# Kernel optimization log

Hardware: AMD Instinct MI355X
Metric: run time of the kernel (lower is better)

## Reference

```python
import jax, jax.numpy as jnp
import numpy as np


def _grid_sample_points(feat, gx, gy):
    """Bilinear grid_sample at point list, align_corners=False, zeros padding.
    feat: [B, H, W, C]; gx, gy: [B, N] normalized coords in [-1, 1].
    Returns [B, N, C].
    """
    B, H, W, C = feat.shape
    # unnormalize (align_corners=False): -1 -> -0.5, +1 -> size-0.5
    ix = (gx + 1.0) * (W * 0.5) - 0.5
    iy = (gy + 1.0) * (H * 0.5) - 0.5
    x0 = jnp.floor(ix)
    y0 = jnp.floor(iy)
    x1 = x0 + 1.0
    y1 = y0 + 1.0
    wx1 = ix - x0
    wx0 = 1.0 - wx1
    wy1 = iy - y0
    wy0 = 1.0 - wy1
    bidx = jnp.arange(B)[:, None]  # [B,1] broadcasts against [B,N]

    def gather(yy, xx):
        valid = (xx >= 0) & (xx <= W - 1) & (yy >= 0) & (yy <= H - 1)
        xi = jnp.clip(xx, 0, W - 1).astype(jnp.int32)
        yi = jnp.clip(yy, 0, H - 1).astype(jnp.int32)
        v = feat[bidx, yi, xi]  # [B, N, C]
        return v * valid[..., None].astype(feat.dtype)

    out = (gather(y0, x0) * (wy0 * wx0)[..., None]
           + gather(y0, x1) * (wy0 * wx1)[..., None]
           + gather(y1, x0) * (wy1 * wx0)[..., None]
           + gather(y1, x1) * (wy1 * wx1)[..., None])
    return out


def setup_inputs() -> dict:
    key = jax.random.key(0)
    k1, k2, k3, k4, k5 = jax.random.split(key, 5)
    B, C, T, Wd, Hd = 16, 64, 16, 36, 36
    N, D = 4096, C * T  # num_neurons, num_input
    x = jax.random.normal(k1, (B, C, T, Wd, Hd), dtype=jnp.float32)
    mu = jax.random.uniform(k2, (N, 2), minval=-1.0, maxval=1.0, dtype=jnp.float32)
    sigma = jax.random.uniform(k3, (N,), dtype=jnp.float32)  # unused in eval mode
    W = jax.random.normal(k4, (N, D), dtype=jnp.float32) * 0.02
    b = jax.random.normal(k5, (N,), dtype=jnp.float32) * 0.01
    return {"x": x, "mu": mu, "sigma": sigma, "W": W, "b": b}


def reference(x, mu, sigma, W, b):
    # eval-mode forward (self.training == False): grid = mu broadcast over batch
    B, C, T, Wd, Hd = x.shape
    N = mu.shape[0]
    # torch: x.view(B, C*T, Wd, Hd); grid_sample treats dim2 as H_in, dim3 as W_in
    feat = x.reshape(B, C * T, Wd, Hd).transpose(0, 2, 3, 1)
    g = jnp.clip(mu, -1.0, 1.0)
    gx = jnp.broadcast_to(g[:, 0], (B, N))  # grid[...,0] indexes W_in
    gy = jnp.broadcast_to(g[:, 1], (B, N))  # grid[...,1] indexes H_in
    sampled = _grid_sample_points(feat, gx, gy)  # [B, N, C*T]
    # PoissonLinearReadout 3D path == per-neuron dot product (diagonal of full matmul)
    y = jnp.einsum('bnc,nc->bn', sampled, W) + b
    return jax.nn.elu(y) + 1.0
```

## Files before the change

kernel.cpp:

```cpp
#include <hip/hip_runtime.h>
#include <hip/hip_bf16.h>
#include <cmath>

#define CT    1024
#define PIX   1296
#define BATCH 16
#define NNEUR 4096
#define HW    36
#define NBINS (HW * HW)
#define NB    4
#define BQ    4
#define BCT   (BATCH * CT)

#if defined(__has_builtin)
#  if __has_builtin(__builtin_amdgcn_fdot2_f32_bf16)
#    define HAVE_FDOT2_BF16 1
#  endif
#endif
#ifndef HAVE_FDOT2_BF16
#  define HAVE_FDOT2_BF16 0
#endif

typedef __bf16 bf16x2 __attribute__((ext_vector_type(2)));
__device__ __forceinline__ bf16x2 as_bf16x2(unsigned u) {
    union { unsigned u; bf16x2 v; } cv; cv.u = u; return cv.v;
}

__device__ __forceinline__ unsigned short bfu(float f) {
    __hip_bfloat16 h = __float2bfloat16(f);
    return *reinterpret_cast<unsigned short*>(&h);
}
__device__ __forceinline__ float bflo(unsigned u) { return __uint_as_float(u << 16); }
__device__ __forceinline__ float bfhi(unsigned u) { return __uint_as_float(u & 0xFFFF0000u); }

__global__ __launch_bounds__(256) void transpose_bf16_kernel(
    const float* __restrict__ x, __hip_bfloat16* __restrict__ feat)
{
    __shared__ unsigned short lds[64][34];
    const int b      = blockIdx.z;
    const int ctBase = blockIdx.y * 64;
    const int pBase  = blockIdx.x * 32;
    const int t      = threadIdx.x;
    const size_t xb  = (size_t)b * CT * PIX;
    {
        const int r  = t >> 2;
        const int pc = (t & 3) * 8;
        const float* src = x + xb + (size_t)(ctBase + r) * PIX + pBase + pc;
        if (pBase + 32 <= PIX) {
            float4 a = reinterpret_cast<const float4*>(src)[0];
            float4 c = reinterpret_cast<const float4*>(src)[1];
            lds[r][pc + 0] = bfu(a.x); lds[r][pc + 1] = bfu(a.y);
            lds[r][pc + 2] = bfu(a.z); lds[r][pc + 3] = bfu(a.w);
            lds[r][pc + 4] = bfu(c.x); lds[r][pc + 5] = bfu(c.y);
            lds[r][pc + 6] = bfu(c.z); lds[r][pc + 7] = bfu(c.w);
        } else {
#pragma unroll
            for (int i = 0; i < 8; ++i) {
                int p = pBase + pc + i;
                lds[r][pc + i] = (p < PIX) ? bfu(src[i]) : (unsigned short)0;
            }
        }
    }
    __syncthreads();
    const int pr = t >> 3;
    const int cc = (t & 7) * 8;
    if (pBase + pr < PIX) {
        unsigned short o[8];
#pragma unroll
        for (int i = 0; i < 8; ++i) o[i] = lds[cc + i][pr];
        const size_t off = ((size_t)(pBase + pr) * BATCH + b) * CT + ctBase + cc;
        *reinterpret_cast<uint4*>((unsigned short*)feat + off) = *reinterpret_cast<uint4*>(o);
    }
}

__global__ __launch_bounds__(1024) void sortpack_kernel(
    const float* __restrict__ mu, int* __restrict__ perm,
    const float* __restrict__ W, __hip_bfloat16* __restrict__ Wb)
{
    const int t = threadIdx.x;
    if (blockIdx.x != 0) {
        const int i = (blockIdx.x - 1) * 1024 + t;
        const float4 v = reinterpret_cast<const float4*>(W)[i];
        unsigned short o[4] = { bfu(v.x), bfu(v.y), bfu(v.z), bfu(v.w) };
        reinterpret_cast<ushort4*>(Wb)[i] = *reinterpret_cast<ushort4*>(o);
        return;
    }

    __shared__ int hist[NBINS];
    __shared__ int chunkSum[48];
    for (int i = t; i < NBINS; i += 1024) hist[i] = 0;
    __syncthreads();

    int key[4];
#pragma unroll
    for (int j = 0; j < 4; ++j) {
        const int n = t + j * 1024;
        float gx = fminf(fmaxf(mu[2 * n],     -1.f), 1.f);
        float gy = fminf(fmaxf(mu[2 * n + 1], -1.f), 1.f);
        float ix = (gx + 1.f) * (HW * 0.5f) - 0.5f;
        float iy = (gy + 1.f) * (HW * 0.5f) - 0.5f;
        int xi = min(max((int)floorf(ix), 0), HW - 1);
        int yi = min(max((int)floorf(iy), 0), HW - 1);
        key[j] = yi * HW + xi;
        atomicAdd(&hist[key[j]], 1);
    }
    __syncthreads();
    if (t < 41) {
        int s = 0;
        for (int i = 0; i < 32; ++i) {
            int idx = t * 32 + i;
            if (idx < NBINS) s += hist[idx];
        }
        chunkSum[t] = s;
    }
    __syncthreads();
    if (t == 0) {
        int run = 0;
        for (int i = 0; i < 41; ++i) { int v = chunkSum[i]; chunkSum[i] = run; run += v; }
    }
    __syncthreads();
    if (t < 41) {
        int run = chunkSum[t];
        for (int i = 0; i < 32; ++i) {
            int idx = t * 32 + i;
            if (idx < NBINS) { int v = hist[idx]; hist[idx] = run; run += v; }
        }
    }
    __syncthreads();
#pragma unroll
    for (int j = 0; j < 4; ++j) {
        const int n = t + j * 1024;
        const int pos = atomicAdd(&hist[key[j]], 1);
        perm[pos] = n;
    }
}

__global__ __launch_bounds__(256) void readout_bf16_kernel(
    const __hip_bfloat16* __restrict__ feat,
    const float* __restrict__ mu,
    const __hip_bfloat16* __restrict__ Wb,
    const float* __restrict__ bias,
    const int* __restrict__ perm,
    float* __restrict__ out)
{
    const int bid = blockIdx.x;
    const int xcd = bid & 7;
    const int r   = bid >> 3;
    const int g   = xcd * 128 + (r >> 2);
    const int q   = r & 3;
    const int t = threadIdx.x;
    const int c = t & 127;
    const int h = t >> 7;

    const int4 nids = *reinterpret_cast<const int4*>(perm + g * NB);
    const int nid[NB] = { nids.x, nids.y, nids.z, nids.w };

    uint4 wq[NB];
#pragma unroll
    for (int nb = 0; nb < NB; ++nb)
        wq[nb] = reinterpret_cast<const uint4*>(Wb + (size_t)nid[nb] * CT)[c];

#if !HAVE_FDOT2_BF16
    float w[NB][8];
#pragma unroll
    for (int nb = 0; nb < NB; ++nb) {
        w[nb][0] = bflo(wq[nb].x); w[nb][1] = bfhi(wq[nb].x);
        w[nb][2] = bflo(wq[nb].y); w[nb][3] = bfhi(wq[nb].y);
        w[nb][4] = bflo(wq[nb].z); w[nb][5] = bfhi(wq[nb].z);
        w[nb][6] = bflo(wq[nb].w); w[nb][7] = bfhi(wq[nb].w);
    }
#endif

    __shared__ float wmat16[16][NB];
    __shared__ int   upix[16];
    __shared__ float uw[16][NB];
    __shared__ int   ucount_s;

    if (t < 16) {
#pragma unroll
        for (int j = 0; j < NB; ++j) wmat16[t][j] = 0.f;
    }

    int   mypix = -1;
    float mycw  = 0.f;
    if (t < 16) {
        const int nb = t >> 2, k = t & 3;
        const int n = nid[nb];
        float gx = fminf(fmaxf(mu[2 * n],     -1.f), 1.f);
        float gy = fminf(fmaxf(mu[2 * n + 1], -1.f), 1.f);
        float ix = (gx + 1.f) * (HW * 0.5f) - 0.5f;
        float iy = (gy + 1.f) * (HW * 0.5f) - 0.5f;
        float x0f = floorf(ix), y0f = floorf(iy);
        float wx1 = ix - x0f, wx0 = 1.f - wx1;
        float wy1 = iy - y0f, wy0 = 1.f - wy1;
        int xx = (int)x0f + (k & 1), yy = (int)y0f + (k >> 1);
        bool valid = (xx >= 0) && (xx < HW) && (yy >= 0) && (yy < HW);
        int xi = min(max(xx, 0), HW - 1), yi = min(max(yy, 0), HW - 1);
        mypix = yi * HW + xi;
        mycw  = ((k & 1) ? wx1 : wx0) * ((k >> 1) ? wy1 : wy0) * (valid ? 1.f : 0.f);
    }

    int myslot = 15;
#pragma unroll
    for (int j = 15; j >= 0; --j) {
        int pj = __shfl(mypix, j, 64);
        if (pj == mypix) myslot = j;
    }
    if (t < 16) atomicAdd(&wmat16[myslot][t >> 2], mycw);

    const bool uniq = (t < 16) && (myslot == t);
    const unsigned long long mask = __ballot(uniq);
    if (t == 0) ucount_s = __popcll(mask);
    const int pix0 = __shfl(mypix, 0, 64);
    __syncthreads();

    const int U    = ucount_s;
    const int Upad = (U + 3) & ~3;
    if (uniq) {
        const int pos = __popcll(mask & ((1ull << t) - 1));
        upix[pos] = mypix;
#pragma unroll
        for (int j = 0; j < NB; ++j) uw[pos][j] = wmat16[t][j];
    }
    if (t >= U && t < Upad) {
        upix[t] = pix0;
#pragma unroll
        for (int j = 0; j < NB; ++j) uw[t][j] = 0.f;
    }
    __syncthreads();

    float acc[NB][2];
#pragma unroll
    for (int nb = 0; nb < NB; ++nb) { acc[nb][0] = 0.f; acc[nb][1] = 0.f; }

    const int b0 = q * BQ + h * 2;
    const unsigned short* fb = (const unsigned short*)feat + (size_t)b0 * CT + (size_t)c * 8;

    for (int u = 0; u < Upad; u += 4) {
        int poff[4];
#pragma unroll
        for (int s = 0; s < 4; ++s) poff[s] = upix[u + s] * BCT;
        uint4 va[4], vb[4];
#pragma unroll
        for (int s = 0; s < 4; ++s) {
            va[s] = *reinterpret_cast<const uint4*>(fb + poff[s]);
            vb[s] = *reinterpret_cast<const uint4*>(fb + poff[s] + CT);
        }
#pragma unroll
        for (int s = 0; s < 4; ++s) {
            const float4 pw = *reinterpret_cast<const float4*>(uw[u + s]);
            const float pws[NB] = { pw.x, pw.y, pw.z, pw.w };
#if HAVE_FDOT2_BF16
#pragma unroll
            for (int nb = 0; nb < NB; ++nb) {
                if (pws[nb] != 0.f) {
                    float d0 = __builtin_amdgcn_fdot2_f32_bf16(as_bf16x2(va[s].x), as_bf16x2(wq[nb].x), 0.f, false);
                    float d1 = __builtin_amdgcn_fdot2_f32_bf16(as_bf16x2(vb[s].x), as_bf16x2(wq[nb].x), 0.f, false);
                    d0 = __builtin_amdgcn_fdot2_f32_bf16(as_bf16x2(va[s].y), as_bf16x2(wq[nb].y), d0, false);
                    d1 = __builtin_amdgcn_fdot2_f32_bf16(as_bf16x2(vb[s].y), as_bf16x2(wq[nb].y), d1, false);
                    d0 = __builtin_amdgcn_fdot2_f32_bf16(as_bf16x2(va[s].z), as_bf16x2(wq[nb].z), d0, false);
                    d1 = __builtin_amdgcn_fdot2_f32_bf16(as_bf16x2(vb[s].z), as_bf16x2(wq[nb].z), d1, false);
                    d0 = __builtin_amdgcn_fdot2_f32_bf16(as_bf16x2(va[s].w), as_bf16x2(wq[nb].w), d0, false);
                    d1 = __builtin_amdgcn_fdot2_f32_bf16(as_bf16x2(vb[s].w), as_bf16x2(wq[nb].w), d1, false);
                    acc[nb][0] = fmaf(pws[nb], d0, acc[nb][0]);
                    acc[nb][1] = fmaf(pws[nb], d1, acc[nb][1]);
                }
            }
#else
            float fa[8] = { bflo(va[s].x), bfhi(va[s].x), bflo(va[s].y), bfhi(va[s].y),
                            bflo(va[s].z), bfhi(va[s].z), bflo(va[s].w), bfhi(va[s].w) };
            float fbv[8] = { bflo(vb[s].x), bfhi(vb[s].x), bflo(vb[s].y), bfhi(vb[s].y),
                             bflo(vb[s].z), bfhi(vb[s].z), bflo(vb[s].w), bfhi(vb[s].w) };
#pragma unroll
            for (int nb = 0; nb < NB; ++nb) {
                if (pws[nb] != 0.f) {
                    float d0 = fa[0]  * w[nb][0];
                    float d1 = fbv[0] * w[nb][0];
#pragma unroll
                    for (int j = 1; j < 8; ++j) {
                        d0 = fmaf(fa[j],  w[nb][j], d0);
                        d1 = fmaf(fbv[j], w[nb][j], d1);
                    }
                    acc[nb][0] = fmaf(pws[nb], d0, acc[nb][0]);
                    acc[nb][1] = fmaf(pws[nb], d1, acc[nb][1]);
                }
            }
#endif
        }
    }

    __shared__ float red[4][NB][2];
#pragma unroll
    for (int nb = 0; nb < NB; ++nb) {
#pragma unroll
        for (int i = 0; i < 2; ++i) {
            float v = acc[nb][i];
#pragma unroll
            for (int off = 32; off > 0; off >>= 1)
                v += __shfl_down(v, off, 64);
            acc[nb][i] = v;
        }
    }
    const int wave = t >> 6, lane = t & 63;
    if (lane == 0) {
#pragma unroll
        for (int nb = 0; nb < NB; ++nb) {
            red[wave][nb][0] = acc[nb][0];
            red[wave][nb][1] = acc[nb][1];
        }
    }
    __syncthreads();
    if (t < NB * BQ) {
        const int nb = t >> 2, bl = t & 3;
        const int hh = bl >> 1, i = bl & 1;
        float y = red[hh * 2][nb][i] + red[hh * 2 + 1][nb][i] + bias[nid[nb]];
        const int b = q * BQ + bl;
        out[(size_t)b * NNEUR + nid[nb]] = (y > 0.f) ? (y + 1.f) : expf(y);
    }
}

__global__ __launch_bounds__(256) void readout_f32_strided_kernel(
    const float* __restrict__ x,
    const float* __restrict__ mu,
    const float* __restrict__ Wm,
    const float* __restrict__ bias,
    float* __restrict__ out)
{
    const int n = blockIdx.x;
    const int t = threadIdx.x;
    const float4 w4 = reinterpret_cast<const float4*>(Wm + (size_t)n * CT)[t];
    float gx = fminf(fmaxf(mu[2 * n],     -1.f), 1.f);
    float gy = fminf(fmaxf(mu[2 * n + 1], -1.f), 1.f);
    float ix = (gx + 1.f) * (HW * 0.5f) - 0.5f;
    float iy = (gy + 1.f) * (HW * 0.5f) - 0.5f;
    float x0f = floorf(ix), y0f = floorf(iy);
    float wx1 = ix - x0f, wx0 = 1.f - wx1;
    float wy1 = iy - y0f, wy0 = 1.f - wy1;
    int x0 = (int)x0f, y0 = (int)y0f;
    float cw[4]; int cp[4];
#pragma unroll
    for (int k = 0; k < 4; ++k) {
        int xx = x0 + (k & 1), yy = y0 + (k >> 1);
        bool valid = (xx >= 0) && (xx < HW) && (yy >= 0) && (yy < HW);
        int xi = min(max(xx, 0), HW - 1), yi = min(max(yy, 0), HW - 1);
        cp[k] = yi * HW + xi;
        cw[k] = ((k & 1) ? wx1 : wx0) * ((k >> 1) ? wy1 : wy0) * (valid ? 1.f : 0.f);
    }
    float acc[BATCH];
#pragma unroll
    for (int b = 0; b < BATCH; ++b) {
        float s = 0.f;
#pragma unroll
        for (int k = 0; k < 4; ++k) {
            if (cw[k] != 0.f) {
                const float* fp = x + (size_t)b * CT * PIX + cp[k];
                const int c0 = 4 * t;
                s += cw[k] * (fp[(size_t)(c0 + 0) * PIX] * w4.x
                            + fp[(size_t)(c0 + 1) * PIX] * w4.y
                            + fp[(size_t)(c0 + 2) * PIX] * w4.z
                            + fp[(size_t)(c0 + 3) * PIX] * w4.w);
            }
        }
        acc[b] = s;
    }
#pragma unroll
    for (int b = 0; b < BATCH; ++b) {
        float v = acc[b];
#pragma unroll
        for (int off = 32; off > 0; off >>= 1)
            v += __shfl_down(v, off, 64);
        acc[b] = v;
    }
    __shared__ float red[4][BATCH];
    const int wave = t >> 6, lane = t & 63;
    if (lane == 0) {
#pragma unroll
        for (int b = 0; b < BATCH; ++b) red[wave][b] = acc[b];
    }
    __syncthreads();
    if (t < BATCH) {
        float y = red[0][t] + red[1][t] + red[2][t] + red[3][t] + bias[n];
        out[(size_t)t * NNEUR + n] = (y > 0.f) ? (y + 1.f) : expf(y);
    }
}

extern "C" void kernel_launch(void* const* d_in, const int* in_sizes, int n_in,
                              void* d_out, int out_size, void* d_ws, size_t ws_size,
                              hipStream_t stream)
{
    const float* x    = (const float*)d_in[0];
    const float* mu   = (const float*)d_in[1];
    const float* Wm   = (const float*)d_in[3];
    const float* bias = (const float*)d_in[4];
    float* out = (float*)d_out;

    const size_t featBytes = (size_t)BATCH * PIX * CT * sizeof(__hip_bfloat16);
    const size_t wBytes    = (size_t)NNEUR * CT * sizeof(__hip_bfloat16);
    const size_t permBytes = (size_t)NNEUR * sizeof(int);
    if (ws_size >= featBytes + wBytes + permBytes) {
        __hip_bfloat16* feat = (__hip_bfloat16*)d_ws;
        __hip_bfloat16* Wb   = (__hip_bfloat16*)((char*)d_ws + featBytes);
        int* perm = (int*)((char*)d_ws + featBytes + wBytes);
        dim3 tg((PIX + 31) / 32, CT / 64, BATCH);
        transpose_bf16_kernel<<<tg, 256, 0, stream>>>(x, feat);
        sortpack_kernel<<<1 + NNEUR * CT / 4 / 1024, 1024, 0, stream>>>(mu, perm, Wm, Wb);
        readout_bf16_kernel<<<(NNEUR / NB) * (BATCH / BQ), 256, 0, stream>>>(
            feat, mu, Wb, bias, perm, out);
    } else {
        readout_f32_strided_kernel<<<NNEUR, 256, 0, stream>>>(x, mu, Wm, bias, out);
    }
}
```

Measured before the change: 58.71 us.

## Merge transpose and sort/pack into one staging kernel, deepen readout load batching

Combines the feature transpose, the neuron bin-sort and the W bf16 pack into a single launch of 256-thread blocks, with a flat block index choosing the role. This drops one kernel launch and lets the three stages run on the GPU at the same time. The readout kernel now batches 8 unique pixels per iteration instead of 4, padding U to a multiple of 8, so more loads are in flight, and gets a launch_bounds occupancy hint. The costs are higher register pressure, some wasted loads on zero-weight padding slots, and a serial sort block that now runs with only 256 threads and 16 keys each.

Result: faster. 57.28 us, median of 2 (-2.4%).

```diff
diff --git a/kernel.cpp b/kernel.cpp
--- a/kernel.cpp
+++ b/kernel.cpp
@@ -12,6 +12,11 @@
 #define BQ    4
 #define BCT   (BATCH * CT)
 
+#define SORT_BLK   1
+#define PACK_BLKS  2048
+#define TRAN_BLKS  (41 * 16 * 16)
+#define STAGE_GRID (SORT_BLK + PACK_BLKS + TRAN_BLKS)
+
 #if defined(__has_builtin)
 #  if __has_builtin(__builtin_amdgcn_fdot2_f32_bf16)
 #    define HAVE_FDOT2_BF16 1
@@ -25,7 +30,6 @@
 __device__ __forceinline__ bf16x2 as_bf16x2(unsigned u) {
     union { unsigned u; bf16x2 v; } cv; cv.u = u; return cv.v;
 }
-
 __device__ __forceinline__ unsigned short bfu(float f) {
     __hip_bfloat16 h = __float2bfloat16(f);
     return *reinterpret_cast<unsigned short*>(&h);
@@ -33,14 +37,81 @@
 __device__ __forceinline__ float bflo(unsigned u) { return __uint_as_float(u << 16); }
 __device__ __forceinline__ float bfhi(unsigned u) { return __uint_as_float(u & 0xFFFF0000u); }
 
-__global__ __launch_bounds__(256) void transpose_bf16_kernel(
-    const float* __restrict__ x, __hip_bfloat16* __restrict__ feat)
+__global__ __launch_bounds__(256) void stage_kernel(
+    const float* __restrict__ x, __hip_bfloat16* __restrict__ feat,
+    const float* __restrict__ mu, int* __restrict__ perm,
+    const float* __restrict__ W, __hip_bfloat16* __restrict__ Wb)
 {
+    const int bid = blockIdx.x;
+    const int t   = threadIdx.x;
+
+    __shared__ int hist[NBINS];
+    __shared__ int chunkSum[48];
     __shared__ unsigned short lds[64][34];
-    const int b      = blockIdx.z;
-    const int ctBase = blockIdx.y * 64;
-    const int pBase  = blockIdx.x * 32;
-    const int t      = threadIdx.x;
+
+    if (bid == 0) {
+        for (int i = t; i < NBINS; i += 256) hist[i] = 0;
+        __syncthreads();
+        int key[16];
+#pragma unroll
+        for (int j = 0; j < 16; ++j) {
+            const int n = t * 16 + j;
+            float gx = fminf(fmaxf(mu[2 * n],     -1.f), 1.f);
+            float gy = fminf(fmaxf(mu[2 * n + 1], -1.f), 1.f);
+            float ix = (gx + 1.f) * (HW * 0.5f) - 0.5f;
+            float iy = (gy + 1.f) * (HW * 0.5f) - 0.5f;
+            int xi = min(max((int)floorf(ix), 0), HW - 1);
+            int yi = min(max((int)floorf(iy), 0), HW - 1);
+            key[j] = yi * HW + xi;
+            atomicAdd(&hist[key[j]], 1);
+        }
+        __syncthreads();
+        if (t < 41) {
+            int s = 0;
+            for (int i = 0; i < 32; ++i) {
+                int idx = t * 32 + i;
+                if (idx < NBINS) s += hist[idx];
+            }
+            chunkSum[t] = s;
+        }
+        __syncthreads();
+        if (t == 0) {
+            int run = 0;
+            for (int i = 0; i < 41; ++i) { int v = chunkSum[i]; chunkSum[i] = run; run += v; }
+        }
+        __syncthreads();
+        if (t < 41) {
+            int run = chunkSum[t];
+            for (int i = 0; i < 32; ++i) {
+                int idx = t * 32 + i;
+                if (idx < NBINS) { int v = hist[idx]; hist[idx] = run; run += v; }
+            }
+        }
+        __syncthreads();
+#pragma unroll
+        for (int j = 0; j < 16; ++j) {
+            const int n = t * 16 + j;
+            const int pos = atomicAdd(&hist[key[j]], 1);
+            perm[pos] = n;
+        }
+        return;
+    }
+
+    if (bid <= PACK_BLKS) {
+        const size_t i = ((size_t)(bid - 1) * 256 + t) * 2;
+        const float4 a = reinterpret_cast<const float4*>(W)[i];
+        const float4 b = reinterpret_cast<const float4*>(W)[i + 1];
+        unsigned short o[8] = { bfu(a.x), bfu(a.y), bfu(a.z), bfu(a.w),
+                                bfu(b.x), bfu(b.y), bfu(b.z), bfu(b.w) };
+        reinterpret_cast<uint4*>((unsigned short*)Wb)[((size_t)(bid - 1) * 256 + t)] =
+            *reinterpret_cast<uint4*>(o);
+        return;
+    }
+
+    const int flat   = bid - 1 - PACK_BLKS;
+    const int pBase  = (flat % 41) * 32;
+    const int ctBase = ((flat / 41) % 16) * 64;
+    const int b      = flat / (41 * 16);
     const size_t xb  = (size_t)b * CT * PIX;
     {
         const int r  = t >> 2;
@@ -73,69 +144,7 @@
     }
 }
 
-__global__ __launch_bounds__(1024) void sortpack_kernel(
-    const float* __restrict__ mu, int* __restrict__ perm,
-    const float* __restrict__ W, __hip_bfloat16* __restrict__ Wb)
-{
-    const int t = threadIdx.x;
-    if (blockIdx.x != 0) {
-        const int i = (blockIdx.x - 1) * 1024 + t;
-        const float4 v = reinterpret_cast<const float4*>(W)[i];
-        unsigned short o[4] = { bfu(v.x), bfu(v.y), bfu(v.z), bfu(v.w) };
-        reinterpret_cast<ushort4*>(Wb)[i] = *reinterpret_cast<ushort4*>(o);
-        return;
-    }
-
-    __shared__ int hist[NBINS];
-    __shared__ int chunkSum[48];
-    for (int i = t; i < NBINS; i += 1024) hist[i] = 0;
-    __syncthreads();
-
-    int key[4];
-#pragma unroll
-    for (int j = 0; j < 4; ++j) {
-        const int n = t + j * 1024;
-        float gx = fminf(fmaxf(mu[2 * n],     -1.f), 1.f);
-        float gy = fminf(fmaxf(mu[2 * n + 1], -1.f), 1.f);
-        float ix = (gx + 1.f) * (HW * 0.5f) - 0.5f;
-        float iy = (gy + 1.f) * (HW * 0.5f) - 0.5f;
-        int xi = min(max((int)floorf(ix), 0), HW - 1);
-        int yi = min(max((int)floorf(iy), 0), HW - 1);
-        key[j] = yi * HW + xi;
-        atomicAdd(&hist[key[j]], 1);
-    }
-    __syncthreads();
-    if (t < 41) {
-        int s = 0;
-        for (int i = 0; i < 32; ++i) {
-            int idx = t * 32 + i;
-            if (idx < NBINS) s += hist[idx];
-        }
-        chunkSum[t] = s;
-    }
-    __syncthreads();
-    if (t == 0) {
-        int run = 0;
-        for (int i = 0; i < 41; ++i) { int v = chunkSum[i]; chunkSum[i] = run; run += v; }
-    }
-    __syncthreads();
-    if (t < 41) {
-        int run = chunkSum[t];
-        for (int i = 0; i < 32; ++i) {
-            int idx = t * 32 + i;
-            if (idx < NBINS) { int v = hist[idx]; hist[idx] = run; run += v; }
-        }
-    }
-    __syncthreads();
-#pragma unroll
-    for (int j = 0; j < 4; ++j) {
-        const int n = t + j * 1024;
-        const int pos = atomicAdd(&hist[key[j]], 1);
-        perm[pos] = n;
-    }
-}
-
-__global__ __launch_bounds__(256) void readout_bf16_kernel(
+__global__ __launch_bounds__(256, 4) void readout_bf16_kernel(
     const __hip_bfloat16* __restrict__ feat,
     const float* __restrict__ mu,
     const __hip_bfloat16* __restrict__ Wb,
@@ -215,7 +224,7 @@
     __syncthreads();
 
     const int U    = ucount_s;
-    const int Upad = (U + 3) & ~3;
+    const int Upad = (U + 7) & ~7;
     if (uniq) {
         const int pos = __popcll(mask & ((1ull << t) - 1));
         upix[pos] = mypix;
@@ -236,18 +245,18 @@
     const int b0 = q * BQ + h * 2;
     const unsigned short* fb = (const unsigned short*)feat + (size_t)b0 * CT + (size_t)c * 8;
 
-    for (int u = 0; u < Upad; u += 4) {
-        int poff[4];
-#pragma unroll
-        for (int s = 0; s < 4; ++s) poff[s] = upix[u + s] * BCT;
-        uint4 va[4], vb[4];
-#pragma unroll
-        for (int s = 0; s < 4; ++s) {
+    for (int u = 0; u < Upad; u += 8) {
+        int poff[8];
+#pragma unroll
+        for (int s = 0; s < 8; ++s) poff[s] = upix[u + s] * BCT;
+        uint4 va[8], vb[8];
+#pragma unroll
+        for (int s = 0; s < 8; ++s) {
             va[s] = *reinterpret_cast<const uint4*>(fb + poff[s]);
             vb[s] = *reinterpret_cast<const uint4*>(fb + poff[s] + CT);
         }
 #pragma unroll
-        for (int s = 0; s < 4; ++s) {
+        for (int s = 0; s < 8; ++s) {
             const float4 pw = *reinterpret_cast<const float4*>(uw[u + s]);
             const float pws[NB] = { pw.x, pw.y, pw.z, pw.w };
 #if HAVE_FDOT2_BF16
@@ -401,9 +410,7 @@
         __hip_bfloat16* feat = (__hip_bfloat16*)d_ws;
         __hip_bfloat16* Wb   = (__hip_bfloat16*)((char*)d_ws + featBytes);
         int* perm = (int*)((char*)d_ws + featBytes + wBytes);
-        dim3 tg((PIX + 31) / 32, CT / 64, BATCH);
-        transpose_bf16_kernel<<<tg, 256, 0, stream>>>(x, feat);
-        sortpack_kernel<<<1 + NNEUR * CT / 4 / 1024, 1024, 0, stream>>>(mu, perm, Wm, Wb);
+        stage_kernel<<<STAGE_GRID, 256, 0, stream>>>(x, feat, mu, perm, Wm, Wb);
         readout_bf16_kernel<<<(NNEUR / NB) * (BATCH / BQ), 256, 0, stream>>>(
             feat, mu, Wb, bias, perm, out);
     } else {
```
